# Kernel tuning notes

Hardware: AMD Instinct MI355X
Metric: run time of the kernel (lower is better)

Reference implementation:

```python
import jax, jax.numpy as jnp
import numpy as np

N = 50000          # atoms (nodes)
NEIGH = 12         # neighbors per atom
N_CRYS = 500       # crystals, 100 atoms each (contiguous)
H_E = 128          # h_fea_edge
H_A = 128          # h_fea_angle
N_CLS = 2
BOND_STEPS, BOND_MIN, BOND_MAX = 40, 0.0, 8.0
ANG_STEPS, ANG_MIN, ANG_MAX = 8, -1.0, 1.0


def _gbf(data, dmin, dmax, steps):
    # Gaussian basis expansion on the last (new) axis
    filters = jnp.linspace(dmin, dmax, steps, dtype=jnp.float32)
    gamma = (dmax - dmin) / steps
    return jnp.exp(-((data[..., None] - filters) ** 2) / (gamma ** 2))


def _sage_conv(x, src, dst, Wl, Wr, b):
    # PyG SAGEConv, mean aggregation:
    #   out_i = Wl @ mean_{(j->i) in E} x_j + b + Wr @ x_i
    n = x.shape[0]
    msg = x[src]                                             # [E, F] gather
    agg = jax.ops.segment_sum(msg, dst, num_segments=n)      # [N, F] scatter-add
    cnt = jax.ops.segment_sum(jnp.ones((src.shape[0],), x.dtype), dst, num_segments=n)
    agg = agg / jnp.maximum(cnt, 1.0)[:, None]
    return agg @ Wl.T + b + x @ Wr.T


def _segment_mean_pool(x, crys_idx):
    # crys_idx: [C, 2] contiguous [start, end) ranges covering [0, N)
    n = x.shape[0]
    starts = crys_idx[:, 0]
    seg_id = jnp.searchsorted(starts, jnp.arange(n), side='right') - 1
    counts = (crys_idx[:, 1] - crys_idx[:, 0]).astype(x.dtype)
    summed = jax.ops.segment_sum(x, seg_id, num_segments=crys_idx.shape[0])
    return summed / jnp.maximum(counts, 1.0)[:, None]


def setup_inputs() -> dict:
    key = jax.random.key(0)
    ks = jax.random.split(key, 24)
    in_b = BOND_STEPS * NEIGH            # 480
    in_a = ANG_STEPS * NEIGH * NEIGH     # 1152
    h_cat = H_E + H_A                    # 256

    def lin(k, fo, fi):
        return jax.random.normal(k, (fo, fi), jnp.float32) * (1.0 / np.sqrt(fi))

    atoms_per = N // N_CRYS
    starts = np.arange(N_CRYS, dtype=np.int32) * atoms_per
    crys_idx = jnp.asarray(np.stack([starts, starts + atoms_per], axis=1))

    return {
        'bond_fea': jax.random.uniform(ks[0], (N, NEIGH), jnp.float32) * BOND_MAX,
        'angle_fea': jax.random.uniform(ks[1], (N, NEIGH, NEIGH), jnp.float32) * 2.0 - 1.0,
        'species': jax.random.randint(ks[2], (N,), 0, 100, jnp.int32),
        'nbr_idx': jax.random.randint(ks[3], (N, NEIGH), 0, N, jnp.int32),
        'crys_idx': crys_idx,
        'Wl_b1': lin(ks[4], H_E, in_b), 'Wr_b1': lin(ks[5], H_E, in_b),
        'b_b1': jnp.zeros((H_E,), jnp.float32),
        'Wl_a1': lin(ks[6], H_A, in_a), 'Wr_a1': lin(ks[7], H_A, in_a),
        'b_a1': jnp.zeros((H_A,), jnp.float32),
        'Wl_b': jnp.stack([lin(ks[8], H_E, H_E), lin(ks[9], H_E, H_E)]),
        'Wr_b': jnp.stack([lin(ks[10], H_E, H_E), lin(ks[11], H_E, H_E)]),
        'b_b': jnp.zeros((2, H_E), jnp.float32),
        'Wl_a': jnp.stack([lin(ks[12], H_A, H_A), lin(ks[13], H_A, H_A)]),
        'Wr_a': jnp.stack([lin(ks[14], H_A, H_A), lin(ks[15], H_A, H_A)]),
        'b_a': jnp.zeros((2, H_A), jnp.float32),
        'W_mlp': jnp.stack([lin(ks[16], h_cat, h_cat), lin(ks[17], h_cat, h_cat)]),
        'b_mlp': jnp.zeros((2, h_cat), jnp.float32),
        'W_fc': lin(ks[18], N_CLS, h_cat),
        'b_fc': jnp.zeros((N_CLS,), jnp.float32),
    }


def reference(bond_fea, angle_fea, species, nbr_idx, crys_idx,
              Wl_b1, Wr_b1, b_b1, Wl_a1, Wr_a1, b_a1,
              Wl_b, Wr_b, b_b, Wl_a, Wr_a, b_a,
              W_mlp, b_mlp, W_fc, b_fc):
    n, neigh = nbr_idx.shape
    # get_edge_index: source = repeated node id, dest = neighbor id
    src = jnp.repeat(jnp.arange(n, dtype=nbr_idx.dtype), neigh)   # [N*neigh]
    dst = nbr_idx.reshape(-1)                                     # [N*neigh]

    # GBF expansions, flattened per node
    edge_fea = _gbf(bond_fea, BOND_MIN, BOND_MAX, BOND_STEPS).reshape(n, -1)    # [N, 480]
    ang_fea = _gbf(angle_fea, ANG_MIN, ANG_MAX, ANG_STEPS).reshape(n, -1)       # [N, 1152]

    # first SAGE layers (dropout_prob = 0 -> identity)
    b_out = jax.nn.relu(_sage_conv(edge_fea, src, dst, Wl_b1, Wr_b1, b_b1))
    a_out = jax.nn.relu(_sage_conv(ang_fea, src, dst, Wl_a1, Wr_a1, b_a1))

    # stacked SAGE layers (n_conv - 1 = 2 each)
    for i in range(Wl_b.shape[0]):
        b_out = jax.nn.relu(_sage_conv(b_out, src, dst, Wl_b[i], Wr_b[i], b_b[i]))
    for i in range(Wl_a.shape[0]):
        a_out = jax.nn.relu(_sage_conv(a_out, src, dst, Wl_a[i], Wr_a[i], b_a[i]))

    crys_fea = jnp.concatenate([b_out, a_out], axis=1)   # [N, 256]
    crys_fea = _segment_mean_pool(crys_fea, crys_idx)     # [C, 256]

    for i in range(W_mlp.shape[0]):
        crys_fea = crys_fea @ W_mlp[i].T + b_mlp[i]

    return crys_fea @ W_fc.T + b_fc                       # [C, n_classification]
```

## Files before the change

### kernel.cpp

```cpp
#include <hip/hip_runtime.h>

typedef _Float16 f16;
typedef _Float16 f16x8 __attribute__((ext_vector_type(8)));
typedef float f32x4 __attribute__((ext_vector_type(4)));

#define N_ATOMS 50000
#define NEIGH   12
#define NEDGE   (N_ATOMS * NEIGH)
#define NCRYS   500
#define NBLK    196

__device__ __forceinline__ void gld_lds16(const void* g, void* l) {
  __builtin_amdgcn_global_load_lds(
      (const __attribute__((address_space(1))) unsigned int*)g,
      (__attribute__((address_space(3))) unsigned int*)l, 16, 0, 0);
}

typedef f16 AsT[2][4][256][8];
typedef f16 BsT[2][4][128][8];

template <int MODE, int K>
__device__ __forceinline__ void gemm1_body(
    const float* __restrict__ Asrc, const f16* __restrict__ Wcat,
    f16* __restrict__ P, f16* __restrict__ Q, int n, AsT& As, BsT& Bs) {
  const int tid = threadIdx.x;
  const int lane = tid & 63;
  const int wid = tid >> 6;
  const int wr = wid >> 1;
  const int wc = wid & 1;
  const int row0 = blockIdx.x * 256;
  const int half = blockIdx.y;
  const f16* Wh = Wcat + (size_t)half * 128 * K;
  f16* outp = half ? Q : P;

  const int bcol = tid & 127;
  const int bkb = tid >> 7;
  const int sArow = tid & 255;
  const int sAkb0 = tid >> 8;
  int arow = row0 + sArow;
  if (arow >= n) arow = n - 1;

  f32x4 acc[4][4];
#pragma unroll
  for (int m = 0; m < 4; ++m)
#pragma unroll
    for (int q = 0; q < 4; ++q) acc[m][q] = (f32x4)0.f;

  auto stage = [&](int buf, int k0) {
    gld_lds16(Wh + (size_t)bcol * K + k0 + bkb * 8, &Bs[buf][bkb][bcol][0]);
#pragma unroll
    for (int p = 0; p < 2; ++p) {
      int kb = sAkb0 + 2 * p;
      int kg0 = k0 + kb * 8;
      f16 v[8];
      if constexpr (MODE == 1) {
        int jn = kg0 / 40;
        int kk0 = kg0 - jn * 40;
        float d = Asrc[arow * NEIGH + jn];
#pragma unroll
        for (int j = 0; j < 8; ++j) {
          float t = d - (kk0 + j) * (8.0f / 39.0f);
          v[j] = (f16)__expf(-t * t * 25.0f);
        }
      } else {
        int jn = kg0 >> 3;
        float d = Asrc[arow * 144 + jn];
#pragma unroll
        for (int j = 0; j < 8; ++j) {
          float t = d - (-1.0f + j * (2.0f / 7.0f));
          v[j] = (f16)__expf(-t * t * 16.0f);
        }
      }
      *(f16x8*)&As[buf][kb][sArow][0] = *(const f16x8*)v;
    }
  };

  constexpr int NT = K / 32;
  stage(0, 0);
  __syncthreads();
  int buf = 0;
  for (int t = 0; t < NT; ++t) {
    if (t + 1 < NT) stage(buf ^ 1, (t + 1) * 32);
    const int kb = lane >> 4;
    const int r16 = lane & 15;
    f16x8 a[4], b[4];
#pragma unroll
    for (int m = 0; m < 4; ++m)
      a[m] = *(const f16x8*)&As[buf][kb][wr * 64 + m * 16 + r16][0];
#pragma unroll
    for (int q = 0; q < 4; ++q)
      b[q] = *(const f16x8*)&Bs[buf][kb][wc * 64 + q * 16 + r16][0];
#pragma unroll
    for (int m = 0; m < 4; ++m)
#pragma unroll
      for (int q = 0; q < 4; ++q)
        acc[m][q] =
            __builtin_amdgcn_mfma_f32_16x16x32_f16(a[m], b[q], acc[m][q], 0, 0, 0);
    __syncthreads();
    buf ^= 1;
  }

  const int crow = (lane >> 4) * 4;
  const int ccol = lane & 15;
#pragma unroll
  for (int m = 0; m < 4; ++m) {
#pragma unroll
    for (int r = 0; r < 4; ++r) {
      int row = row0 + wr * 64 + m * 16 + crow + r;
      if (row < n) {
#pragma unroll
        for (int q = 0; q < 4; ++q)
          outp[(size_t)row * 128 + wc * 64 + q * 16 + ccol] = (f16)acc[m][q][r];
      }
    }
  }
}

__global__ __launch_bounds__(512) void gemm1all(
    const float* __restrict__ angle, const f16* __restrict__ Wa,
    f16* __restrict__ Pa, f16* __restrict__ Qa,
    const float* __restrict__ bond, const f16* __restrict__ Wb,
    f16* __restrict__ Pb, f16* __restrict__ Qb, int n) {
  __shared__ __align__(16) AsT As;
  __shared__ __align__(16) BsT Bs;
  if (blockIdx.z == 0)
    gemm1_body<2, 1152>(angle, Wa, Pa, Qa, n, As, Bs);
  else
    gemm1_body<1, 480>(bond, Wb, Pb, Qb, n, As, Bs);
}

__global__ __launch_bounds__(512) void gemmL(
    f16* __restrict__ axb, f16* __restrict__ axa, const f16* __restrict__ Wall,
    const float* __restrict__ bb, const float* __restrict__ ba, int lidx, int n) {
  __shared__ __align__(16) AsT As;
  __shared__ __align__(16) BsT Bs;
  const int path = blockIdx.y;
  f16* ax = path ? axa : axb;
  const f16* W = Wall + (size_t)(path * 2 + lidx) * 32768;
  const float* bias = (path ? ba : bb) + lidx * 128;

  const int tid = threadIdx.x;
  const int lane = tid & 63;
  const int wid = tid >> 6;
  const int wr = wid >> 1;
  const int wc = wid & 1;
  const int row0 = blockIdx.x * 256;

  const int bcol = tid & 127;
  const int bkb = tid >> 7;
  const int sArow = tid & 255;
  const int sAkb0 = tid >> 8;
  int arow = row0 + sArow;
  if (arow >= n) arow = n - 1;

  f32x4 acc[4][4];
#pragma unroll
  for (int m = 0; m < 4; ++m)
#pragma unroll
    for (int q = 0; q < 4; ++q) acc[m][q] = (f32x4)0.f;

  auto stage = [&](int buf, int k0) {
    gld_lds16(W + (size_t)bcol * 256 + k0 + bkb * 8, &Bs[buf][bkb][bcol][0]);
#pragma unroll
    for (int p = 0; p < 2; ++p) {
      int kb = sAkb0 + 2 * p;
      gld_lds16(ax + (size_t)arow * 256 + k0 + kb * 8, &As[buf][kb][sArow][0]);
    }
  };

  stage(0, 0);
  __syncthreads();
  int buf = 0;
  for (int t = 0; t < 8; ++t) {
    if (t + 1 < 8) stage(buf ^ 1, (t + 1) * 32);
    const int kb = lane >> 4;
    const int r16 = lane & 15;
    f16x8 a[4], b[4];
#pragma unroll
    for (int m = 0; m < 4; ++m)
      a[m] = *(const f16x8*)&As[buf][kb][wr * 64 + m * 16 + r16][0];
#pragma unroll
    for (int q = 0; q < 4; ++q)
      b[q] = *(const f16x8*)&Bs[buf][kb][wc * 64 + q * 16 + r16][0];
#pragma unroll
    for (int m = 0; m < 4; ++m)
#pragma unroll
      for (int q = 0; q < 4; ++q)
        acc[m][q] =
            __builtin_amdgcn_mfma_f32_16x16x32_f16(a[m], b[q], acc[m][q], 0, 0, 0);
    __syncthreads();
    buf ^= 1;
  }

  const int crow = (lane >> 4) * 4;
  const int ccol = lane & 15;
#pragma unroll
  for (int m = 0; m < 4; ++m) {
#pragma unroll
    for (int r = 0; r < 4; ++r) {
      int row = row0 + wr * 64 + m * 16 + crow + r;
      if (row < n) {
#pragma unroll
        for (int q = 0; q < 4; ++q) {
          int col = wc * 64 + q * 16 + ccol;
          float v = acc[m][q][r] + bias[col];
          ax[(size_t)row * 256 + 128 + col] = (f16)fmaxf(v, 0.0f);
        }
      }
    }
  }
}

__global__ void cvtW(const float* __restrict__ Wl, const float* __restrict__ Wr,
                     f16* __restrict__ outp, int K) {
  int c = blockIdx.y;
  int k = blockIdx.x * 256 + threadIdx.x;
  if (k < K)
    outp[(size_t)c * K + k] =
        (f16)((c < 128) ? Wl[(size_t)c * K + k] : Wr[(size_t)(c - 128) * K + k]);
}

__global__ void cvtW_small(const float* __restrict__ Wl_b, const float* __restrict__ Wr_b,
                           const float* __restrict__ Wl_a, const float* __restrict__ Wr_a,
                           f16* __restrict__ outp) {
  int idx = blockIdx.x * 256 + threadIdx.x;
  int l = idx >> 15;
  int c = (idx >> 8) & 127;
  int k = idx & 255;
  const float* Wl = (l < 2) ? Wl_b + (size_t)l * 16384 : Wl_a + (size_t)(l - 2) * 16384;
  const float* Wr = (l < 2) ? Wr_b + (size_t)l * 16384 : Wr_a + (size_t)(l - 2) * 16384;
  float v = (k < 128) ? Wl[(size_t)c * 128 + k] : Wr[(size_t)c * 128 + (k - 128)];
  outp[idx] = (f16)v;
}

__global__ void k_count(const int* __restrict__ nbr, int* __restrict__ deg) {
  int e = blockIdx.x * 256 + threadIdx.x;
  if (e < NEDGE) atomicAdd(&deg[nbr[e]], 1);
}
__global__ void k_scan1(const int* __restrict__ deg, int* __restrict__ rowptr,
                        int* __restrict__ bsum) {
  __shared__ int s[256];
  int t = threadIdx.x, i = blockIdx.x * 256 + t;
  int v = (i < N_ATOMS) ? deg[i] : 0;
  s[t] = v;
  __syncthreads();
  for (int off = 1; off < 256; off <<= 1) {
    int x = (t >= off) ? s[t - off] : 0;
    __syncthreads();
    s[t] += x;
    __syncthreads();
  }
  if (i < N_ATOMS) rowptr[i] = s[t] - v;
  if (t == 255) bsum[blockIdx.x] = s[255];
}
__global__ void k_scan2(int* __restrict__ bsum) {
  __shared__ int s[256];
  int t = threadIdx.x;
  int v = (t < NBLK) ? bsum[t] : 0;
  s[t] = v;
  __syncthreads();
  for (int off = 1; off < 256; off <<= 1) {
    int x = (t >= off) ? s[t - off] : 0;
    __syncthreads();
    s[t] += x;
    __syncthreads();
  }
  if (t < NBLK) bsum[t] = s[t] - v;
}
__global__ void k_scan3(int* __restrict__ rowptr, const int* __restrict__ bsum) {
  int i = blockIdx.x * 256 + threadIdx.x;
  if (i < N_ATOMS) rowptr[i] += bsum[blockIdx.x];
  if (i == 0) rowptr[N_ATOMS] = NEDGE;
}
__global__ void k_fill(const int* __restrict__ nbr, const int* __restrict__ rowptr,
                       int* __restrict__ cursor, int* __restrict__ eidx) {
  int e = blockIdx.x * 256 + threadIdx.x;
  if (e < NEDGE) {
    int dst = nbr[e];
    int pos = rowptr[dst] + atomicAdd(&cursor[dst], 1);
    eidx[pos] = (e / NEIGH) << 8;
  }
}

__global__ __launch_bounds__(256) void gather_fin1(
    const f16* __restrict__ Pb, const f16* __restrict__ Qb,
    const f16* __restrict__ Pa, const f16* __restrict__ Qa,
    const int* __restrict__ rowptr, const int* __restrict__ eidx,
    const float* __restrict__ bias_b, const float* __restrict__ bias_a,
    f16* __restrict__ axb, f16* __restrict__ axa) {
  const int path = blockIdx.y;
  const char* Pc = (const char*)(path ? Pa : Pb);
  const f16* Q = path ? Qa : Qb;
  const float* bias = path ? bias_a : bias_b;
  f16* ax = path ? axa : axb;
  const int t = threadIdx.x;
  const int a = blockIdx.x * 16 + (t >> 4);
  const int g = (t & 15) * 8;
  const unsigned gb = (unsigned)(t & 15) * 16;
  const int s0 = rowptr[a], s1 = rowptr[a + 1];
  float acc[8];
#pragma unroll
  for (int u = 0; u < 8; ++u) acc[u] = 0.f;
  int j = s0;
  for (; j + 8 <= s1; j += 8) {
    f16x8 v[8];
#pragma unroll
    for (int u = 0; u < 8; ++u)
      v[u] = *(const f16x8*)(Pc + (size_t)((unsigned)eidx[j + u] + gb));
    f16x8 s = ((v[0] + v[1]) + (v[2] + v[3])) + ((v[4] + v[5]) + (v[6] + v[7]));
#pragma unroll
    for (int c = 0; c < 8; ++c) acc[c] += (float)s[c];
  }
  for (; j + 4 <= s1; j += 4) {
    f16x8 v0 = *(const f16x8*)(Pc + (size_t)((unsigned)eidx[j] + gb));
    f16x8 v1 = *(const f16x8*)(Pc + (size_t)((unsigned)eidx[j + 1] + gb));
    f16x8 v2 = *(const f16x8*)(Pc + (size_t)((unsigned)eidx[j + 2] + gb));
    f16x8 v3 = *(const f16x8*)(Pc + (size_t)((unsigned)eidx[j + 3] + gb));
    f16x8 s = (v0 + v1) + (v2 + v3);
#pragma unroll
    for (int c = 0; c < 8; ++c) acc[c] += (float)s[c];
  }
  for (; j < s1; ++j) {
    f16x8 v = *(const f16x8*)(Pc + (size_t)((unsigned)eidx[j] + gb));
#pragma unroll
    for (int c = 0; c < 8; ++c) acc[c] += (float)v[c];
  }
  f16x8 q = *(const f16x8*)&Q[(size_t)a * 128 + g];
  float inv = 1.0f / fmaxf((float)(s1 - s0), 1.0f);
  f16 outv[8];
#pragma unroll
  for (int u = 0; u < 8; ++u) {
    float v = acc[u] * inv + bias[g + u] + (float)q[u];
    outv[u] = (f16)fmaxf(v, 0.0f);
  }
  *(f16x8*)&ax[(size_t)a * 256 + 128 + g] = *(const f16x8*)outv;
}

__global__ __launch_bounds__(256) void gather_mean(
    f16* __restrict__ axb, f16* __restrict__ axa,
    const int* __restrict__ rowptr, const int* __restrict__ eidx) {
  f16* ax = blockIdx.y ? axa : axb;
  const char* axc = (const char*)ax;
  const int t = threadIdx.x;
  const int a = blockIdx.x * 16 + (t >> 4);
  const int g = (t & 15) * 8;
  const unsigned gb = 256u + (unsigned)(t & 15) * 16;
  const int s0 = rowptr[a], s1 = rowptr[a + 1];
  float acc[8];
#pragma unroll
  for (int u = 0; u < 8; ++u) acc[u] = 0.f;
  int j = s0;
  for (; j + 8 <= s1; j += 8) {
    f16x8 v[8];
#pragma unroll
    for (int u = 0; u < 8; ++u)
      v[u] = *(const f16x8*)(axc + (size_t)(((unsigned)eidx[j + u] << 1) + gb));
    f16x8 s = ((v[0] + v[1]) + (v[2] + v[3])) + ((v[4] + v[5]) + (v[6] + v[7]));
#pragma unroll
    for (int c = 0; c < 8; ++c) acc[c] += (float)s[c];
  }
  for (; j + 4 <= s1; j += 4) {
    f16x8 v0 = *(const f16x8*)(axc + (size_t)(((unsigned)eidx[j] << 1) + gb));
    f16x8 v1 = *(const f16x8*)(axc + (size_t)(((unsigned)eidx[j + 1] << 1) + gb));
    f16x8 v2 = *(const f16x8*)(axc + (size_t)(((unsigned)eidx[j + 2] << 1) + gb));
    f16x8 v3 = *(const f16x8*)(axc + (size_t)(((unsigned)eidx[j + 3] << 1) + gb));
    f16x8 s = (v0 + v1) + (v2 + v3);
#pragma unroll
    for (int c = 0; c < 8; ++c) acc[c] += (float)s[c];
  }
  for (; j < s1; ++j) {
    f16x8 v = *(const f16x8*)(axc + (size_t)(((unsigned)eidx[j] << 1) + gb));
#pragma unroll
    for (int c = 0; c < 8; ++c) acc[c] += (float)v[c];
  }
  float inv = 1.0f / fmaxf((float)(s1 - s0), 1.0f);
  f16 outv[8];
#pragma unroll
  for (int u = 0; u < 8; ++u) outv[u] = (f16)(acc[u] * inv);
  *(f16x8*)&ax[(size_t)a * 256 + g] = *(const f16x8*)outv;
}

__global__ __launch_bounds__(256) void head_kernel(
    const f16* __restrict__ axb, const f16* __restrict__ axa,
    const int* __restrict__ crys, const float* __restrict__ W_mlp,
    const float* __restrict__ b_mlp, const float* __restrict__ W_fc,
    const float* __restrict__ b_fc, float* __restrict__ outp) {
  __shared__ float sh0[256], sh1[256];
  const int cry = blockIdx.x, c = threadIdx.x;
  const int s = crys[2 * cry], e = crys[2 * cry + 1];
  const f16* src = (c < 128) ? axb : axa;
  const int ch = c & 127;
  float sum = 0.f;
  for (int r = s; r < e; ++r) sum += (float)src[(size_t)r * 256 + 128 + ch];
  sh0[c] = sum / fmaxf((float)(e - s), 1.0f);
  __syncthreads();
  {
    const float* wrow = W_mlp + (size_t)c * 256;
    float s2 = b_mlp[c];
#pragma unroll 8
    for (int k = 0; k < 256; k += 4) {
      float4 w = *(const float4*)&wrow[k];
      s2 += sh0[k] * w.x + sh0[k + 1] * w.y + sh0[k + 2] * w.z + sh0[k + 3] * w.w;
    }
    sh1[c] = s2;
  }
  __syncthreads();
  {
    const float* wrow = W_mlp + 65536 + (size_t)c * 256;
    float s2 = b_mlp[256 + c];
#pragma unroll 8
    for (int k = 0; k < 256; k += 4) {
      float4 w = *(const float4*)&wrow[k];
      s2 += sh1[k] * w.x + sh1[k + 1] * w.y + sh1[k + 2] * w.z + sh1[k + 3] * w.w;
    }
    sh0[c] = s2;
  }
  __syncthreads();
  if (c < 2) {
    const float* wrow = W_fc + c * 256;
    float s2 = b_fc[c];
    for (int k = 0; k < 256; ++k) s2 += sh0[k] * wrow[k];
    outp[cry * 2 + c] = s2;
  }
}

extern "C" void kernel_launch(void* const* d_in, const int* in_sizes, int n_in,
                              void* d_out, int out_size, void* d_ws, size_t ws_size,
                              hipStream_t stream) {
  const float* bond  = (const float*)d_in[0];
  const float* angle = (const float*)d_in[1];
  const int*   nbr   = (const int*)d_in[3];
  const int*   crys  = (const int*)d_in[4];
  const float* Wl_b1 = (const float*)d_in[5];
  const float* Wr_b1 = (const float*)d_in[6];
  const float* b_b1  = (const float*)d_in[7];
  const float* Wl_a1 = (const float*)d_in[8];
  const float* Wr_a1 = (const float*)d_in[9];
  const float* b_a1  = (const float*)d_in[10];
  const float* Wl_b  = (const float*)d_in[11];
  const float* Wr_b  = (const float*)d_in[12];
  const float* b_b   = (const float*)d_in[13];
  const float* Wl_a  = (const float*)d_in[14];
  const float* Wr_a  = (const float*)d_in[15];
  const float* b_a   = (const float*)d_in[16];
  const float* W_mlp = (const float*)d_in[17];
  const float* b_mlp = (const float*)d_in[18];
  const float* W_fc  = (const float*)d_in[19];
  const float* b_fc  = (const float*)d_in[20];

  char* w = (char*)d_ws;
  auto alloc = [&](size_t bytes) {
    void* p = (void*)w;
    w += (bytes + 255) & ~(size_t)255;
    return p;
  };
  f16* axb = (f16*)alloc((size_t)N_ATOMS * 256 * 2);
  f16* axa = (f16*)alloc((size_t)N_ATOMS * 256 * 2);
  f16* Pb  = (f16*)alloc((size_t)N_ATOMS * 128 * 2);
  f16* Qb  = (f16*)alloc((size_t)N_ATOMS * 128 * 2);
  f16* Pa  = (f16*)alloc((size_t)N_ATOMS * 128 * 2);
  f16* Qa  = (f16*)alloc((size_t)N_ATOMS * 128 * 2);
  f16* Wb1c = (f16*)alloc((size_t)256 * 480 * 2);
  f16* Wa1c = (f16*)alloc((size_t)256 * 1152 * 2);
  f16* Wsm  = (f16*)alloc((size_t)4 * 128 * 256 * 2);
  int* deg    = (int*)alloc((size_t)2 * N_ATOMS * 4);
  int* cursor = deg + N_ATOMS;
  int* rowptr = (int*)alloc((size_t)(N_ATOMS + 1) * 4);
  int* eidx   = (int*)alloc((size_t)NEDGE * 4);
  int* bsum   = (int*)alloc(256 * 4);

  cvtW<<<dim3(2, 256), 256, 0, stream>>>(Wl_b1, Wr_b1, Wb1c, 480);
  cvtW<<<dim3(5, 256), 256, 0, stream>>>(Wl_a1, Wr_a1, Wa1c, 1152);
  cvtW_small<<<512, 256, 0, stream>>>(Wl_b, Wr_b, Wl_a, Wr_a, Wsm);

  hipMemsetAsync(deg, 0, (size_t)2 * N_ATOMS * 4, stream);
  k_count<<<(NEDGE + 255) / 256, 256, 0, stream>>>(nbr, deg);
  k_scan1<<<NBLK, 256, 0, stream>>>(deg, rowptr, bsum);
  k_scan2<<<1, 256, 0, stream>>>(bsum);
  k_scan3<<<NBLK, 256, 0, stream>>>(rowptr, bsum);
  k_fill<<<(NEDGE + 255) / 256, 256, 0, stream>>>(nbr, rowptr, cursor, eidx);

  const int GT = (N_ATOMS + 255) / 256;
  const int AG = N_ATOMS / 16;

  gemm1all<<<dim3(GT, 2, 2), 512, 0, stream>>>(angle, Wa1c, Pa, Qa,
                                               bond, Wb1c, Pb, Qb, N_ATOMS);
  gather_fin1<<<dim3(AG, 2), 256, 0, stream>>>(Pb, Qb, Pa, Qa, rowptr, eidx,
                                               b_b1, b_a1, axb, axa);

  for (int l = 0; l < 2; ++l) {
    gather_mean<<<dim3(AG, 2), 256, 0, stream>>>(axb, axa, rowptr, eidx);
    gemmL<<<dim3(GT, 2), 512, 0, stream>>>(axb, axa, Wsm, b_b, b_a, l, N_ATOMS);
  }

  head_kernel<<<NCRYS, 256, 0, stream>>>(axb, axa, crys, W_mlp, b_mlp, W_fc, b_fc,
                                         (float*)d_out);
}
```

Baseline: 405.4 us.

## Triple-buffer GEMM LDS staging with explicit vmcnt waits and barriers

```diff
diff --git a/kernel.cpp b/kernel.cpp
--- a/kernel.cpp
+++ b/kernel.cpp
@@ -16,8 +16,18 @@
       (__attribute__((address_space(3))) unsigned int*)l, 16, 0, 0);
 }
 
-typedef f16 AsT[2][4][256][8];
-typedef f16 BsT[2][4][128][8];
+typedef f16 AsT[3][4][256][8];
+typedef f16 BsT[3][4][128][8];
+
+#define WAITVM(vm)                                                        \
+  asm volatile("s_waitcnt vmcnt(" #vm ") lgkmcnt(0)" ::: "memory");       \
+  __builtin_amdgcn_sched_barrier(0);                                      \
+  __builtin_amdgcn_s_barrier();                                           \
+  __builtin_amdgcn_sched_barrier(0)
+
+#define ENDBAR                                                            \
+  __builtin_amdgcn_sched_barrier(0);                                      \
+  __builtin_amdgcn_s_barrier()
 
 template <int MODE, int K>
 __device__ __forceinline__ void gemm1_body(
@@ -46,7 +56,8 @@
 #pragma unroll
     for (int q = 0; q < 4; ++q) acc[m][q] = (f32x4)0.f;
 
-  auto stage = [&](int buf, int k0) {
+  auto stage = [&](int buf, int t) {
+    int k0 = t * 32;
     gld_lds16(Wh + (size_t)bcol * K + k0 + bkb * 8, &Bs[buf][bkb][bcol][0]);
 #pragma unroll
     for (int p = 0; p < 2; ++p) {
@@ -59,16 +70,16 @@
         float d = Asrc[arow * NEIGH + jn];
 #pragma unroll
         for (int j = 0; j < 8; ++j) {
-          float t = d - (kk0 + j) * (8.0f / 39.0f);
-          v[j] = (f16)__expf(-t * t * 25.0f);
+          float t2 = d - (kk0 + j) * (8.0f / 39.0f);
+          v[j] = (f16)__expf(-t2 * t2 * 25.0f);
         }
       } else {
         int jn = kg0 >> 3;
         float d = Asrc[arow * 144 + jn];
 #pragma unroll
         for (int j = 0; j < 8; ++j) {
-          float t = d - (-1.0f + j * (2.0f / 7.0f));
-          v[j] = (f16)__expf(-t * t * 16.0f);
+          float t2 = d - (-1.0f + j * (2.0f / 7.0f));
+          v[j] = (f16)__expf(-t2 * t2 * 16.0f);
         }
       }
       *(f16x8*)&As[buf][kb][sArow][0] = *(const f16x8*)v;
@@ -77,10 +88,17 @@
 
   constexpr int NT = K / 32;
   stage(0, 0);
-  __syncthreads();
-  int buf = 0;
+  stage(1, 1);
   for (int t = 0; t < NT; ++t) {
-    if (t + 1 < NT) stage(buf ^ 1, (t + 1) * 32);
+    if (t + 2 < NT) stage((t + 2) % 3, t + 2);
+    if (t < NT - 2) {
+      WAITVM(2);
+    } else if (t == NT - 2) {
+      WAITVM(1);
+    } else {
+      WAITVM(0);
+    }
+    const int buf = t % 3;
     const int kb = lane >> 4;
     const int r16 = lane & 15;
     f16x8 a[4], b[4];
@@ -96,8 +114,7 @@
       for (int q = 0; q < 4; ++q)
         acc[m][q] =
             __builtin_amdgcn_mfma_f32_16x16x32_f16(a[m], b[q], acc[m][q], 0, 0, 0);
-    __syncthreads();
-    buf ^= 1;
+    ENDBAR;
   }
 
   const int crow = (lane >> 4) * 4;
@@ -159,7 +176,8 @@
 #pragma unroll
     for (int q = 0; q < 4; ++q) acc[m][q] = (f32x4)0.f;
 
-  auto stage = [&](int buf, int k0) {
+  auto stage = [&](int buf, int t) {
+    int k0 = t * 32;
     gld_lds16(W + (size_t)bcol * 256 + k0 + bkb * 8, &Bs[buf][bkb][bcol][0]);
 #pragma unroll
     for (int p = 0; p < 2; ++p) {
@@ -169,10 +187,17 @@
   };
 
   stage(0, 0);
-  __syncthreads();
-  int buf = 0;
+  stage(1, 1);
   for (int t = 0; t < 8; ++t) {
-    if (t + 1 < 8) stage(buf ^ 1, (t + 1) * 32);
+    if (t + 2 < 8) stage((t + 2) % 3, t + 2);
+    if (t < 6) {
+      WAITVM(6);
+    } else if (t == 6) {
+      WAITVM(3);
+    } else {
+      WAITVM(0);
+    }
+    const int buf = t % 3;
     const int kb = lane >> 4;
     const int r16 = lane & 15;
     f16x8 a[4], b[4];
@@ -188,8 +213,7 @@
       for (int q = 0; q < 4; ++q)
         acc[m][q] =
             __builtin_amdgcn_mfma_f32_16x16x32_f16(a[m], b[q], acc[m][q], 0, 0, 0);
-    __syncthreads();
-    buf ^= 1;
+    ENDBAR;
   }
 
   const int crow = (lane >> 4) * 4;
```

Result: no change. 403.9 us (-0.4%).
